# Kernel tuning notes

Measured on AMD Instinct MI355X. Metric: run time of the kernel, lower is better.

## Reference

```python
import jax, jax.numpy as jnp
import numpy as np

N = 50000          # nodes
E = 400000         # edges (avg degree 8)
F_IN = 128
F_OUT = 128
H = 4
C = F_OUT // H     # 32
SCALE = np.sqrt(C).astype(np.float32)
EPS = 1e-5


def _linear_params(key, fan_out, fan_in):
    # torch nn.Linear default init: U(-1/sqrt(fan_in), 1/sqrt(fan_in))
    bound = 1.0 / np.sqrt(fan_in)
    kw, kb = jax.random.split(key)
    W = jax.random.uniform(kw, (fan_out, fan_in), minval=-bound, maxval=bound, dtype=jnp.float32)
    b = jax.random.uniform(kb, (fan_out,), minval=-bound, maxval=bound, dtype=jnp.float32)
    return W, b


def setup_inputs() -> dict:
    key = jax.random.key(0)
    ks = jax.random.split(key, 12)
    Wq, bq = _linear_params(ks[0], F_OUT, F_IN)
    Wk, bk = _linear_params(ks[1], F_OUT, F_IN)
    Wv, bv = _linear_params(ks[2], F_OUT, F_IN)
    We, be = _linear_params(ks[3], F_OUT, F_IN)
    Wev, bev = _linear_params(ks[4], F_OUT, F_IN)
    Wout, bout = _linear_params(ks[5], F_OUT, F_OUT)
    node_feats = jax.random.normal(ks[6], (N, F_IN), dtype=jnp.float32)
    edge_feats = jax.random.normal(ks[7], (E, F_IN), dtype=jnp.float32)
    src = jax.random.randint(ks[8], (E,), 0, N, dtype=jnp.int32)
    dst = jax.random.randint(ks[9], (E,), 0, N, dtype=jnp.int32)
    return {
        'node_feats': node_feats, 'edge_feats': edge_feats,
        'src': src, 'dst': dst,
        'Wq': Wq, 'bq': bq, 'Wk': Wk, 'bk': bk, 'Wv': Wv, 'bv': bv,
        'We': We, 'be': be, 'Wev': Wev, 'bev': bev, 'Wout': Wout, 'bout': bout,
        'ln_ng': jnp.ones((F_OUT,), jnp.float32), 'ln_nb': jnp.zeros((F_OUT,), jnp.float32),
        'ln_eg': jnp.ones((F_OUT,), jnp.float32), 'ln_eb': jnp.zeros((F_OUT,), jnp.float32),
    }


def _layernorm(x, g, b):
    mu = jnp.mean(x, axis=-1, keepdims=True)
    var = jnp.var(x, axis=-1, keepdims=True)
    return (x - mu) * jax.lax.rsqrt(var + EPS) * g + b


def reference(node_feats, edge_feats, src, dst,
              Wq, bq, Wk, bk, Wv, bv, We, be, Wev, bev, Wout, bout,
              ln_ng, ln_nb, ln_eg, ln_eb):
    # per-node projections, viewed as [N, H, C]
    q = (node_feats @ Wq.T + bq).reshape(N, H, C)
    k = (node_feats @ Wk.T + bk).reshape(N, H, C)
    v = (node_feats @ Wv.T + bv).reshape(N, H, C)
    e = (edge_feats @ We.T + be).reshape(E, H, C)

    # u_dot_v('q','k','score'): per-edge per-head dot -> [E, H, 1]
    score = jnp.einsum('ehc,ehc->eh', q[src], k[dst])[:, :, None]
    m = score / SCALE + e                       # broadcast -> [E, H, C]
    # NOTE: faithful to original — softmax over the HEADS axis (dim=1)
    attn = jax.nn.softmax(m, axis=1)            # [E, H, C]

    # u_mul_e + sum aggregation at destination
    msg = v[src] * attn                         # [E, H, C]
    agg = jax.ops.segment_sum(msg, dst, num_segments=N)   # [N, H, C]

    x = agg.reshape(N, H * C)
    y = m.reshape(E, H * C)
    x = jax.nn.silu(_layernorm(x, ln_ng, ln_nb))
    y = jax.nn.silu(_layernorm(y, ln_eg, ln_eb))
    # residual
    x = (node_feats @ Wout.T + bout) + x
    y = (edge_feats @ Wev.T + bev) + y
    return (x, y)
```

## Files before the change

kernel.cpp:

```cpp
#include <hip/hip_runtime.h>
#include <math.h>

#define NN 50000
#define NE 400000
#define FDIM 128

constexpr float INV_SCALE = 0.17677669529663687f;
constexpr float LN_EPS = 1e-5f;

typedef short bf16x8 __attribute__((ext_vector_type(8)));
typedef float f32x4 __attribute__((ext_vector_type(4)));

static __device__ __forceinline__ short f2bf(float f) {
    unsigned u = __builtin_bit_cast(unsigned, f);
    u += 0x7FFFu + ((u >> 16) & 1u);
    return (short)(u >> 16);
}

static __device__ __forceinline__ void stage_tile(const float* __restrict__ gsrc,
                                                  short* At, int limit, int m0, int tid) {
#pragma unroll
    for (int j = 0; j < 4; ++j) {
        int row = (tid >> 4) + j * 16;
        int g   = tid & 15;
        int m   = m0 + row;
        float4 a0 = make_float4(0.f, 0.f, 0.f, 0.f);
        float4 a1 = make_float4(0.f, 0.f, 0.f, 0.f);
        if (m < limit) {
            const float4* p = (const float4*)(gsrc + (size_t)m * FDIM + g * 8);
            a0 = p[0];
            a1 = p[1];
        }
        bf16x8 h;
        h[0] = f2bf(a0.x); h[1] = f2bf(a0.y); h[2] = f2bf(a0.z); h[3] = f2bf(a0.w);
        h[4] = f2bf(a1.x); h[5] = f2bf(a1.y); h[6] = f2bf(a1.z); h[7] = f2bf(a1.w);
        *(bf16x8*)(At + row * FDIM + ((g ^ (row & 7)) * 8)) = h;
    }
}

static __device__ __forceinline__ void load_afrags(const short* At, int w, int l, bf16x8* a) {
    int lr = l & 15, lq = l >> 4;
    int arow = w * 16 + lr;
#pragma unroll
    for (int ks = 0; ks < 4; ++ks) {
        int ch = ks * 4 + lq;
        a[ks] = *(const bf16x8*)(At + arow * FDIM + ((ch ^ (arow & 7)) * 8));
    }
}

static __device__ __forceinline__ void mfma_gemm(const bf16x8* a,
                                                 const short* __restrict__ W,
                                                 const float* __restrict__ bias,
                                                 int lr, int lq, f32x4* acc) {
#pragma unroll
    for (int n = 0; n < 8; ++n) {
        float bb = bias[n * 16 + lr];
        f32x4 t; t[0] = bb; t[1] = bb; t[2] = bb; t[3] = bb;
        acc[n] = t;
#pragma unroll
        for (int ks = 0; ks < 4; ++ks) {
            bf16x8 b = *(const bf16x8*)(W + (n * 16 + lr) * FDIM + ks * 32 + lq * 8);
            acc[n] = __builtin_amdgcn_mfma_f32_16x16x32_bf16(a[ks], b, acc[n], 0, 0, 0);
        }
    }
}

__global__ __launch_bounds__(256) void convert_weights(
    const float* __restrict__ w0, const float* __restrict__ w1,
    const float* __restrict__ w2, const float* __restrict__ w3,
    const float* __restrict__ w4, const float* __restrict__ w5,
    short* __restrict__ out) {
    int idx = blockIdx.x * 256 + threadIdx.x;
    const float* srcs[6] = {w0, w1, w2, w3, w4, w5};
    out[idx] = f2bf(srcs[idx >> 14][idx & 16383]);
}

__global__ __launch_bounds__(256) void node_proj_kernel(
    const float* __restrict__ nf,
    const short* __restrict__ wq16, const short* __restrict__ wk16,
    const short* __restrict__ wv16, const short* __restrict__ wo16,
    const float* __restrict__ bq, const float* __restrict__ bk,
    const float* __restrict__ bv, const float* __restrict__ bo,
    float* __restrict__ q, float* __restrict__ k, float* __restrict__ v,
    float* __restrict__ xout) {
    __shared__ __align__(16) short At[64 * FDIM];
    int m0  = blockIdx.x * 64;
    int tid = threadIdx.x;
    stage_tile(nf, At, NN, m0, tid);
    __syncthreads();
    int w = tid >> 6, l = tid & 63;
    int lr = l & 15, lq = l >> 4;
    bf16x8 a[4];
    load_afrags(At, w, l, a);
    f32x4 acc[8];
    const short* Ws[4] = {wq16, wk16, wv16, wo16};
    const float* Bs[4] = {bq, bk, bv, bo};
    float*       Os[4] = {q, k, v, xout};
#pragma unroll
    for (int t = 0; t < 4; ++t) {
        mfma_gemm(a, Ws[t], Bs[t], lr, lq, acc);
#pragma unroll
        for (int n = 0; n < 8; ++n)
#pragma unroll
            for (int r = 0; r < 4; ++r) {
                int m = m0 + w * 16 + lq * 4 + r;
                if (m < NN) Os[t][(size_t)m * FDIM + n * 16 + lr] = acc[n][r];
            }
    }
}

__global__ __launch_bounds__(256) void edge_kernel(
    const float* __restrict__ ef, const int* __restrict__ src, const int* __restrict__ dst,
    const short* __restrict__ we16, const short* __restrict__ wev16,
    const float* __restrict__ be, const float* __restrict__ bev,
    const float* __restrict__ q, const float* __restrict__ k, const float* __restrict__ v,
    const float* __restrict__ ln_eg, const float* __restrict__ ln_eb,
    float* __restrict__ agg, float* __restrict__ yout) {
    __shared__ __align__(16) short At[64 * FDIM];
    __shared__ __align__(16) float sc[64 * 4];
    int e0  = blockIdx.x * 64;
    int tid = threadIdx.x;
    stage_tile(ef, At, NE, e0, tid);

    int w = tid >> 6, l = tid & 63;
    {
        int eidx = w * 16 + (l >> 2);
        int h    = l & 3;
        int eg   = e0 + eidx;
        int se = src[eg], de = dst[eg];
        const float4* qp = (const float4*)(q + (size_t)se * FDIM + h * 32);
        const float4* kp = (const float4*)(k + (size_t)de * FDIM + h * 32);
        float s = 0.f;
#pragma unroll
        for (int i = 0; i < 8; ++i) {
            float4 qa = qp[i], ka = kp[i];
            s += qa.x * ka.x + qa.y * ka.y + qa.z * ka.z + qa.w * ka.w;
        }
        sc[eidx * 4 + h] = s * INV_SCALE;
    }
    __syncthreads();

    int lr = l & 15, lq = l >> 4;
    bf16x8 a[4];
    load_afrags(At, w, l, a);
    f32x4 me[8], mvv[8];
    mfma_gemm(a, we16, be, lr, lq, me);
    mfma_gemm(a, wev16, bev, lr, lq, mvv);

    int rowb = w * 16 + lq * 4;
    float sr[4][4];
#pragma unroll
    for (int r = 0; r < 4; ++r) {
        f32x4 t = *(const f32x4*)(sc + (rowb + r) * 4);
        sr[r][0] = t[0]; sr[r][1] = t[1]; sr[r][2] = t[2]; sr[r][3] = t[3];
    }
#pragma unroll
    for (int n = 0; n < 8; ++n)
#pragma unroll
        for (int r = 0; r < 4; ++r)
            me[n][r] += sr[r][n >> 1];

#pragma unroll
    for (int r = 0; r < 4; ++r) {
        int eg = e0 + rowb + r;
        int se = src[eg], de = dst[eg];
#pragma unroll
        for (int half = 0; half < 2; ++half) {
            float v0 = me[half][r],     v1 = me[half + 2][r];
            float v2 = me[half + 4][r], v3 = me[half + 6][r];
            float mx = fmaxf(fmaxf(v0, v1), fmaxf(v2, v3));
            float x0 = __expf(v0 - mx), x1 = __expf(v1 - mx);
            float x2 = __expf(v2 - mx), x3 = __expf(v3 - mx);
            float inv = 1.f / (x0 + x1 + x2 + x3);
            float at[4] = {x0 * inv, x1 * inv, x2 * inv, x3 * inv};
#pragma unroll
            for (int h = 0; h < 4; ++h) {
                int col = (2 * h + half) * 16 + lr;
                float vv = v[(size_t)se * FDIM + col];
                unsafeAtomicAdd(&agg[(size_t)de * FDIM + col], vv * at[h]);
            }
        }
    }

#pragma unroll
    for (int r = 0; r < 4; ++r) {
        float sum1 = 0.f, sum2 = 0.f;
#pragma unroll
        for (int n = 0; n < 8; ++n) { float t = me[n][r]; sum1 += t; sum2 += t * t; }
#pragma unroll
        for (int off = 1; off < 16; off <<= 1) {
            sum1 += __shfl_xor(sum1, off);
            sum2 += __shfl_xor(sum2, off);
        }
        float mean = sum1 * (1.f / 128.f);
        float var  = sum2 * (1.f / 128.f) - mean * mean;
        float rstd = rsqrtf(var + LN_EPS);
        int eg = e0 + rowb + r;
#pragma unroll
        for (int n = 0; n < 8; ++n) {
            int col = n * 16 + lr;
            float t  = (me[n][r] - mean) * rstd * ln_eg[col] + ln_eb[col];
            float si = t / (1.f + __expf(-t));
            yout[(size_t)eg * FDIM + col] = si + mvv[n][r];
        }
    }
}

__global__ __launch_bounds__(256) void node_epilogue(
    const float* __restrict__ agg,
    const float* __restrict__ ln_ng, const float* __restrict__ ln_nb,
    float* __restrict__ xout) {
    int row = blockIdx.x * 4 + (threadIdx.x >> 6);
    if (row >= NN) return;
    int l = threadIdx.x & 63;
    float2 aa = *(const float2*)(agg + (size_t)row * FDIM + l * 2);
    float sum1 = aa.x + aa.y, sum2 = aa.x * aa.x + aa.y * aa.y;
#pragma unroll
    for (int off = 1; off < 64; off <<= 1) {
        sum1 += __shfl_xor(sum1, off);
        sum2 += __shfl_xor(sum2, off);
    }
    float mean = sum1 * (1.f / 128.f);
    float var  = sum2 * (1.f / 128.f) - mean * mean;
    float rstd = rsqrtf(var + LN_EPS);
    float2 gg = *(const float2*)(ln_ng + l * 2);
    float2 bb = *(const float2*)(ln_nb + l * 2);
    float t0 = (aa.x - mean) * rstd * gg.x + bb.x;
    float t1 = (aa.y - mean) * rstd * gg.y + bb.y;
    float s0 = t0 / (1.f + __expf(-t0));
    float s1 = t1 / (1.f + __expf(-t1));
    float2 o = *(const float2*)(xout + (size_t)row * FDIM + l * 2);
    o.x += s0;
    o.y += s1;
    *(float2*)(xout + (size_t)row * FDIM + l * 2) = o;
}

extern "C" void kernel_launch(void* const* d_in, const int* in_sizes, int n_in,
                              void* d_out, int out_size, void* d_ws, size_t ws_size,
                              hipStream_t stream) {
    const float* nf   = (const float*)d_in[0];
    const float* ef   = (const float*)d_in[1];
    const int*   src  = (const int*)d_in[2];
    const int*   dst  = (const int*)d_in[3];
    const float* Wq   = (const float*)d_in[4];  const float* bq   = (const float*)d_in[5];
    const float* Wk   = (const float*)d_in[6];  const float* bk   = (const float*)d_in[7];
    const float* Wv   = (const float*)d_in[8];  const float* bv   = (const float*)d_in[9];
    const float* We   = (const float*)d_in[10]; const float* be   = (const float*)d_in[11];
    const float* Wev  = (const float*)d_in[12]; const float* bev  = (const float*)d_in[13];
    const float* Wout = (const float*)d_in[14]; const float* bout = (const float*)d_in[15];
    const float* ln_ng = (const float*)d_in[16]; const float* ln_nb = (const float*)d_in[17];
    const float* ln_eg = (const float*)d_in[18]; const float* ln_eb = (const float*)d_in[19];

    float* xout = (float*)d_out;
    float* yout = xout + (size_t)NN * FDIM;

    float* q   = (float*)d_ws;
    float* k   = q + (size_t)NN * FDIM;
    float* v   = k + (size_t)NN * FDIM;
    float* agg = v + (size_t)NN * FDIM;
    short* w16 = (short*)(agg + (size_t)NN * FDIM);
    short* wq16  = w16;
    short* wk16  = w16 + 16384;
    short* wv16  = w16 + 32768;
    short* we16  = w16 + 49152;
    short* wev16 = w16 + 65536;
    short* wo16  = w16 + 81920;

    hipMemsetAsync(agg, 0, (size_t)NN * FDIM * sizeof(float), stream);
    convert_weights<<<384, 256, 0, stream>>>(Wq, Wk, Wv, We, Wev, Wout, w16);
    node_proj_kernel<<<(NN + 63) / 64, 256, 0, stream>>>(
        nf, wq16, wk16, wv16, wo16, bq, bk, bv, bout, q, k, v, xout);
    edge_kernel<<<NE / 64, 256, 0, stream>>>(
        ef, src, dst, we16, wev16, be, bev, q, k, v, ln_eg, ln_eb, agg, yout);
    node_epilogue<<<(NN + 3) / 4, 256, 0, stream>>>(agg, ln_ng, ln_nb, xout);
}
```

Baseline: 887.9 us.

## Sort edges by destination and store q/k/v in bf16 to cut atomics

Adds a histogram, a single-block scan and a scatter pass that build a destination-sorted edge permutation. The edge kernel then walks edges in that order, gathering edge features and writing y rows through the permutation. Attention weights are staged in shared memory so consecutive same-destination messages are summed locally before one atomic per run, instead of one atomic per edge element. q, k and v are stored in bf16 to halve gather traffic. The cost is three extra small kernels, including a serial one-block scan over all nodes, scattered reads and writes for edge rows, and lower precision in the score and message values.

```diff
diff --git a/kernel.cpp b/kernel.cpp
--- a/kernel.cpp
+++ b/kernel.cpp
@@ -16,26 +16,9 @@
     u += 0x7FFFu + ((u >> 16) & 1u);
     return (short)(u >> 16);
 }
-
-static __device__ __forceinline__ void stage_tile(const float* __restrict__ gsrc,
-                                                  short* At, int limit, int m0, int tid) {
-#pragma unroll
-    for (int j = 0; j < 4; ++j) {
-        int row = (tid >> 4) + j * 16;
-        int g   = tid & 15;
-        int m   = m0 + row;
-        float4 a0 = make_float4(0.f, 0.f, 0.f, 0.f);
-        float4 a1 = make_float4(0.f, 0.f, 0.f, 0.f);
-        if (m < limit) {
-            const float4* p = (const float4*)(gsrc + (size_t)m * FDIM + g * 8);
-            a0 = p[0];
-            a1 = p[1];
-        }
-        bf16x8 h;
-        h[0] = f2bf(a0.x); h[1] = f2bf(a0.y); h[2] = f2bf(a0.z); h[3] = f2bf(a0.w);
-        h[4] = f2bf(a1.x); h[5] = f2bf(a1.y); h[6] = f2bf(a1.z); h[7] = f2bf(a1.w);
-        *(bf16x8*)(At + row * FDIM + ((g ^ (row & 7)) * 8)) = h;
-    }
+static __device__ __forceinline__ float bf2f(short h) {
+    unsigned u = ((unsigned)(unsigned short)h) << 16;
+    return __builtin_bit_cast(float, u);
 }
 
 static __device__ __forceinline__ void load_afrags(const short* At, int w, int l, bf16x8* a) {
@@ -75,66 +58,147 @@
     out[idx] = f2bf(srcs[idx >> 14][idx & 16383]);
 }
 
+__global__ __launch_bounds__(256) void hist_kernel(const int* __restrict__ dst,
+                                                   int* __restrict__ hist) {
+    int e = blockIdx.x * 256 + threadIdx.x;
+    if (e < NE) atomicAdd(&hist[dst[e]], 1);
+}
+
+__global__ __launch_bounds__(256) void scan_kernel(const int* __restrict__ hist,
+                                                   int* __restrict__ cursor) {
+    __shared__ int wsum[4];
+    __shared__ int srun;
+    int tid = threadIdx.x;
+    int lane = tid & 63, w = tid >> 6;
+    if (tid == 0) srun = 0;
+    __syncthreads();
+    for (int base = 0; base < NN; base += 256) {
+        int i = base + tid;
+        int v = (i < NN) ? hist[i] : 0;
+        int inc = v;
+#pragma unroll
+        for (int off = 1; off < 64; off <<= 1) {
+            int t = __shfl_up(inc, off);
+            if (lane >= off) inc += t;
+        }
+        if (lane == 63) wsum[w] = inc;
+        __syncthreads();
+        int wo = 0;
+        for (int j = 0; j < w; ++j) wo += wsum[j];
+        int run = srun;
+        if (i < NN) cursor[i] = run + wo + inc - v;
+        __syncthreads();
+        if (tid == 255) srun = run + wo + inc;
+        __syncthreads();
+    }
+}
+
+__global__ __launch_bounds__(256) void scatter_kernel(const int* __restrict__ dst,
+                                                      int* __restrict__ cursor,
+                                                      int* __restrict__ sidx) {
+    int e = blockIdx.x * 256 + threadIdx.x;
+    if (e < NE) sidx[atomicAdd(&cursor[dst[e]], 1)] = e;
+}
+
 __global__ __launch_bounds__(256) void node_proj_kernel(
     const float* __restrict__ nf,
     const short* __restrict__ wq16, const short* __restrict__ wk16,
     const short* __restrict__ wv16, const short* __restrict__ wo16,
     const float* __restrict__ bq, const float* __restrict__ bk,
     const float* __restrict__ bv, const float* __restrict__ bo,
-    float* __restrict__ q, float* __restrict__ k, float* __restrict__ v,
+    short* __restrict__ q, short* __restrict__ k, short* __restrict__ v,
     float* __restrict__ xout) {
     __shared__ __align__(16) short At[64 * FDIM];
     int m0  = blockIdx.x * 64;
     int tid = threadIdx.x;
-    stage_tile(nf, At, NN, m0, tid);
+#pragma unroll
+    for (int j = 0; j < 4; ++j) {
+        int row = (tid >> 4) + j * 16;
+        int g   = tid & 15;
+        int m   = m0 + row;
+        float4 a0 = make_float4(0.f, 0.f, 0.f, 0.f);
+        float4 a1 = make_float4(0.f, 0.f, 0.f, 0.f);
+        if (m < NN) {
+            const float4* p = (const float4*)(nf + (size_t)m * FDIM + g * 8);
+            a0 = p[0]; a1 = p[1];
+        }
+        bf16x8 h;
+        h[0] = f2bf(a0.x); h[1] = f2bf(a0.y); h[2] = f2bf(a0.z); h[3] = f2bf(a0.w);
+        h[4] = f2bf(a1.x); h[5] = f2bf(a1.y); h[6] = f2bf(a1.z); h[7] = f2bf(a1.w);
+        *(bf16x8*)(At + row * FDIM + ((g ^ (row & 7)) * 8)) = h;
+    }
     __syncthreads();
     int w = tid >> 6, l = tid & 63;
     int lr = l & 15, lq = l >> 4;
     bf16x8 a[4];
     load_afrags(At, w, l, a);
     f32x4 acc[8];
-    const short* Ws[4] = {wq16, wk16, wv16, wo16};
-    const float* Bs[4] = {bq, bk, bv, bo};
-    float*       Os[4] = {q, k, v, xout};
-#pragma unroll
-    for (int t = 0; t < 4; ++t) {
+    const short* Ws[3] = {wq16, wk16, wv16};
+    const float* Bs[3] = {bq, bk, bv};
+    short*       Os[3] = {q, k, v};
+#pragma unroll
+    for (int t = 0; t < 3; ++t) {
         mfma_gemm(a, Ws[t], Bs[t], lr, lq, acc);
 #pragma unroll
         for (int n = 0; n < 8; ++n)
 #pragma unroll
             for (int r = 0; r < 4; ++r) {
                 int m = m0 + w * 16 + lq * 4 + r;
-                if (m < NN) Os[t][(size_t)m * FDIM + n * 16 + lr] = acc[n][r];
+                if (m < NN) Os[t][(size_t)m * FDIM + n * 16 + lr] = f2bf(acc[n][r]);
             }
     }
+    mfma_gemm(a, wo16, bo, lr, lq, acc);
+#pragma unroll
+    for (int n = 0; n < 8; ++n)
+#pragma unroll
+        for (int r = 0; r < 4; ++r) {
+            int m = m0 + w * 16 + lq * 4 + r;
+            if (m < NN) xout[(size_t)m * FDIM + n * 16 + lr] = acc[n][r];
+        }
 }
 
 __global__ __launch_bounds__(256) void edge_kernel(
     const float* __restrict__ ef, const int* __restrict__ src, const int* __restrict__ dst,
+    const int* __restrict__ sidx,
     const short* __restrict__ we16, const short* __restrict__ wev16,
     const float* __restrict__ be, const float* __restrict__ bev,
-    const float* __restrict__ q, const float* __restrict__ k, const float* __restrict__ v,
+    const short* __restrict__ qbf, const short* __restrict__ kbf, const short* __restrict__ vbf,
     const float* __restrict__ ln_eg, const float* __restrict__ ln_eb,
     float* __restrict__ agg, float* __restrict__ yout) {
     __shared__ __align__(16) short At[64 * FDIM];
     __shared__ __align__(16) float sc[64 * 4];
+    __shared__ int oL[64], sL[64], dL[64];
     int e0  = blockIdx.x * 64;
     int tid = threadIdx.x;
-    stage_tile(ef, At, NE, e0, tid);
+
+#pragma unroll
+    for (int j = 0; j < 4; ++j) {
+        int row = (tid >> 4) + j * 16;
+        int g   = tid & 15;
+        int o   = sidx[e0 + row];
+        const float4* p = (const float4*)(ef + (size_t)o * FDIM + g * 8);
+        float4 a0 = p[0], a1 = p[1];
+        bf16x8 h;
+        h[0] = f2bf(a0.x); h[1] = f2bf(a0.y); h[2] = f2bf(a0.z); h[3] = f2bf(a0.w);
+        h[4] = f2bf(a1.x); h[5] = f2bf(a1.y); h[6] = f2bf(a1.z); h[7] = f2bf(a1.w);
+        *(bf16x8*)(At + row * FDIM + ((g ^ (row & 7)) * 8)) = h;
+    }
 
     int w = tid >> 6, l = tid & 63;
     {
         int eidx = w * 16 + (l >> 2);
         int h    = l & 3;
-        int eg   = e0 + eidx;
-        int se = src[eg], de = dst[eg];
-        const float4* qp = (const float4*)(q + (size_t)se * FDIM + h * 32);
-        const float4* kp = (const float4*)(k + (size_t)de * FDIM + h * 32);
+        int o    = sidx[e0 + eidx];
+        int se = src[o], de = dst[o];
+        if (h == 0) { oL[eidx] = o; sL[eidx] = se; dL[eidx] = de; }
+        const bf16x8* qp = (const bf16x8*)(qbf + (size_t)se * FDIM + h * 32);
+        const bf16x8* kp = (const bf16x8*)(kbf + (size_t)de * FDIM + h * 32);
         float s = 0.f;
 #pragma unroll
-        for (int i = 0; i < 8; ++i) {
-            float4 qa = qp[i], ka = kp[i];
-            s += qa.x * ka.x + qa.y * ka.y + qa.z * ka.z + qa.w * ka.w;
+        for (int i = 0; i < 4; ++i) {
+            bf16x8 qa = qp[i], ka = kp[i];
+#pragma unroll
+            for (int jj = 0; jj < 8; ++jj) s += bf2f(qa[jj]) * bf2f(ka[jj]);
         }
         sc[eidx * 4 + h] = s * INV_SCALE;
     }
@@ -143,6 +207,8 @@
     int lr = l & 15, lq = l >> 4;
     bf16x8 a[4];
     load_afrags(At, w, l, a);
+    __syncthreads();
+
     f32x4 me[8], mvv[8];
     mfma_gemm(a, we16, be, lr, lq, me);
     mfma_gemm(a, wev16, bev, lr, lq, mvv);
@@ -160,10 +226,9 @@
         for (int r = 0; r < 4; ++r)
             me[n][r] += sr[r][n >> 1];
 
+    short* attnL = At;
 #pragma unroll
     for (int r = 0; r < 4; ++r) {
-        int eg = e0 + rowb + r;
-        int se = src[eg], de = dst[eg];
 #pragma unroll
         for (int half = 0; half < 2; ++half) {
             float v0 = me[half][r],     v1 = me[half + 2][r];
@@ -174,11 +239,8 @@
             float inv = 1.f / (x0 + x1 + x2 + x3);
             float at[4] = {x0 * inv, x1 * inv, x2 * inv, x3 * inv};
 #pragma unroll
-            for (int h = 0; h < 4; ++h) {
-                int col = (2 * h + half) * 16 + lr;
-                float vv = v[(size_t)se * FDIM + col];
-                unsafeAtomicAdd(&agg[(size_t)de * FDIM + col], vv * at[h]);
-            }
+            for (int h = 0; h < 4; ++h)
+                attnL[(rowb + r) * FDIM + (2 * h + half) * 16 + lr] = f2bf(at[h]);
         }
     }
 
@@ -195,14 +257,34 @@
         float mean = sum1 * (1.f / 128.f);
         float var  = sum2 * (1.f / 128.f) - mean * mean;
         float rstd = rsqrtf(var + LN_EPS);
-        int eg = e0 + rowb + r;
+        int orow = oL[rowb + r];
 #pragma unroll
         for (int n = 0; n < 8; ++n) {
             int col = n * 16 + lr;
             float t  = (me[n][r] - mean) * rstd * ln_eg[col] + ln_eb[col];
             float si = t / (1.f + __expf(-t));
-            yout[(size_t)eg * FDIM + col] = si + mvv[n][r];
-        }
+            yout[(size_t)orow * FDIM + col] = si + mvv[n][r];
+        }
+    }
+    __syncthreads();
+
+    {
+        int c  = tid & 127;
+        int hh = tid >> 7;
+        int j0 = hh * 32, j1 = j0 + 32;
+        float acc = 0.f;
+        int cur = dL[j0];
+        for (int j = j0; j < j1; ++j) {
+            int d = dL[j];
+            if (d != cur) {
+                unsafeAtomicAdd(&agg[(size_t)cur * FDIM + c], acc);
+                acc = 0.f; cur = d;
+            }
+            float vv = bf2f(vbf[(size_t)sL[j] * FDIM + c]);
+            float aa = bf2f(attnL[j * FDIM + c]);
+            acc += vv * aa;
+        }
+        unsafeAtomicAdd(&agg[(size_t)cur * FDIM + c], acc);
     }
 }
 
@@ -254,11 +336,15 @@
     float* xout = (float*)d_out;
     float* yout = xout + (size_t)NN * FDIM;
 
-    float* q   = (float*)d_ws;
-    float* k   = q + (size_t)NN * FDIM;
-    float* v   = k + (size_t)NN * FDIM;
-    float* agg = v + (size_t)NN * FDIM;
-    short* w16 = (short*)(agg + (size_t)NN * FDIM);
+    char* ws = (char*)d_ws;
+    short* qbf  = (short*)ws;                                   ws += (size_t)NN * FDIM * 2;
+    short* kbf  = (short*)ws;                                   ws += (size_t)NN * FDIM * 2;
+    short* vbf  = (short*)ws;                                   ws += (size_t)NN * FDIM * 2;
+    float* agg  = (float*)ws;                                   ws += (size_t)NN * FDIM * 4;
+    short* w16  = (short*)ws;                                   ws += (size_t)6 * 16384 * 2;
+    int*   hist = (int*)ws;                                     ws += (size_t)NN * 4;
+    int*   curs = (int*)ws;                                     ws += (size_t)NN * 4;
+    int*   sidx = (int*)ws;                                     ws += (size_t)NE * 4;
     short* wq16  = w16;
     short* wk16  = w16 + 16384;
     short* wv16  = w16 + 32768;
@@ -267,10 +353,14 @@
     short* wo16  = w16 + 81920;
 
     hipMemsetAsync(agg, 0, (size_t)NN * FDIM * sizeof(float), stream);
+    hipMemsetAsync(hist, 0, (size_t)NN * sizeof(int), stream);
     convert_weights<<<384, 256, 0, stream>>>(Wq, Wk, Wv, We, Wev, Wout, w16);
+    hist_kernel<<<(NE + 255) / 256, 256, 0, stream>>>(dst, hist);
+    scan_kernel<<<1, 256, 0, stream>>>(hist, curs);
+    scatter_kernel<<<(NE + 255) / 256, 256, 0, stream>>>(dst, curs, sidx);
     node_proj_kernel<<<(NN + 63) / 64, 256, 0, stream>>>(
-        nf, wq16, wk16, wv16, wo16, bq, bk, bv, bout, q, k, v, xout);
+        nf, wq16, wk16, wv16, wo16, bq, bk, bv, bout, qbf, kbf, vbf, xout);
     edge_kernel<<<NE / 64, 256, 0, stream>>>(
-        ef, src, dst, we16, wev16, be, bev, q, k, v, ln_eg, ln_eb, agg, yout);
+        ef, src, dst, sidx, we16, wev16, be, bev, qbf, kbf, vbf, ln_eg, ln_eb, agg, yout);
     node_epilogue<<<(NN + 3) / 4, 256, 0, stream>>>(agg, ln_ng, ln_nb, xout);
 }
```

Result: slower. 969.3 us (+9.2%).
